# Kernel optimization log

Measured on AMD Instinct MI355X. Metric: run time of the kernel, lower is better.

Reference implementation:

```python
import jax, jax.numpy as jnp
import numpy as np

B, C, H, W = 4, 3, 1024, 1024
RADII = (8, 16, 32, 64)
EPS = 1e-5  # BatchNorm2d default eps


def _box_sum(x, r, s):
    # depthwise all-ones conv (kernel r, stride s, VALID padding) == summed box
    return jax.lax.reduce_window(x, 0.0, jax.lax.add, (1, 1, r, r), (1, 1, s, s), 'VALID')


def _axis_interp_ac(x, n_out, axis):
    # bilinear (align_corners=True) interpolation along one axis
    n_in = x.shape[axis]
    pos = jnp.arange(n_out, dtype=x.dtype) * ((n_in - 1) / max(n_out - 1, 1))
    i0 = jnp.clip(jnp.floor(pos).astype(jnp.int32), 0, n_in - 2)
    w = pos - i0.astype(x.dtype)
    a = jnp.take(x, i0, axis=axis)
    b = jnp.take(x, i0 + 1, axis=axis)
    shape = [1] * x.ndim
    shape[axis] = n_out
    w = w.reshape(shape)
    return a * (1 - w) + b * w


def _resize_ac(x, oh, ow):
    x = _axis_interp_ac(x, oh, 2)
    x = _axis_interp_ac(x, ow, 3)
    return x


def _bn(x, g, b, rm, rv):
    inv = g / jnp.sqrt(rv + EPS)
    return x * inv[None, :, None, None] + (b - rm * inv)[None, :, None, None]


def _forward(guide, src, w1, g1, b1, rm1, rv1, w2, g2, b2, rm2, rv2, w3):
    Hg, Wg = guide.shape[2], guide.shape[3]
    gg = guide * guide
    gs = guide * src
    ones = jnp.ones((1, guide.shape[1], Hg, Wg), guide.dtype)
    stats = []
    for r in RADII:
        s = r // 2
        N = _box_sum(ones, r, s)
        mx = _box_sum(guide, r, s) / N
        my = _box_sum(src, r, s) / N
        cov = _box_sum(gs, r, s) / N - mx * my
        var = _box_sum(gg, r, s) / N - mx * mx
        stats.append((mx, my, cov, var))
    mx1, my1, cov1, var1 = stats[0]
    oh, ow = cov1.shape[2], cov1.shape[3]
    feats = [cov1, var1]
    for (_, _, cov, var) in stats[1:]:
        feats.append(_resize_ac(cov, oh, ow))
        feats.append(_resize_ac(var, oh, ow))
    x = jnp.concatenate(feats, axis=1)  # [B,24,oh,ow]
    x = jax.nn.relu(_bn(jnp.einsum('oc,bchw->bohw', w1, x), g1, b1, rm1, rv1))
    x = jax.nn.relu(_bn(jnp.einsum('oc,bchw->bohw', w2, x), g2, b2, rm2, rv2))
    A = jnp.einsum('oc,bchw->bohw', w3, x)  # [B,3,oh,ow]
    bb = my1 - A * mx1
    mean_A = _resize_ac(A, Hg, Wg)
    mean_b = _resize_ac(bb, Hg, Wg)
    return mean_A * guide + mean_b


def setup_inputs() -> dict:
    key = jax.random.key(0)
    ks = jax.random.split(key, 5)
    f32 = jnp.float32
    return {
        'guide': jax.random.normal(ks[0], (B, C, H, W), f32),
        'src': jax.random.normal(ks[1], (B, C, H, W), f32),
        'w1': jax.random.normal(ks[2], (48, 24), f32) * 0.05,
        'g1': jnp.ones((48,), f32), 'b1': jnp.zeros((48,), f32),
        'rm1': jnp.zeros((48,), f32), 'rv1': jnp.ones((48,), f32),
        'w2': jax.random.normal(ks[3], (48, 48), f32) * 0.05,
        'g2': jnp.ones((48,), f32), 'b2': jnp.zeros((48,), f32),
        'rm2': jnp.zeros((48,), f32), 'rv2': jnp.ones((48,), f32),
        'w3': jax.random.normal(ks[4], (3, 48), f32) * 0.05,
    }


def reference(guide, src, w1, g1, b1, rm1, rv1, w2, g2, b2, rm2, rv2, w3):
    return _forward(guide, src, w1, g1, b1, rm1, rv1, w2, g2, b2, rm2, rv2, w3)
```

## Files before the change

kernel.cpp:

```cpp
#include <hip/hip_runtime.h>

typedef float v2f __attribute__((ext_vector_type(2)));

#define HH 1024
#define WW 1024
#define NB 4
#define NC 3
#define BC 12
#define N1 255
#define N2 127
#define N3 63
#define N4 31
#define EPS 1e-5f
#define NPIX (NB * N1 * N1)

constexpr size_t S8_OFF = 0;
constexpr size_t S8_SZ  = 4ull * BC * N1 * N1;
constexpr size_t CV16_OFF = S8_OFF + S8_SZ;
constexpr size_t CV16_SZ  = 2ull * BC * N2 * N2;
constexpr size_t CV32_OFF = CV16_OFF + CV16_SZ;
constexpr size_t CV32_SZ  = 2ull * BC * N3 * N3;
constexpr size_t CV64_OFF = CV32_OFF + CV32_SZ;
constexpr size_t CV64_SZ  = 2ull * BC * N4 * N4;
constexpr size_t AB_OFF = CV64_OFF + CV64_SZ;
constexpr size_t AB_SZ  = 2ull * NB * NC * N1 * N1;
constexpr size_t IB_OFF = AB_OFF + AB_SZ;

__global__ __launch_bounds__(256) void base_kernel(
    const float* __restrict__ guide, const float* __restrict__ src,
    float4* __restrict__ S8q)
{
    __shared__ float smem[8][WW];

    int b  = blockIdx.x % 64;
    int bc = blockIdx.x / 64;
    int t  = threadIdx.x;

    const float* gbase = guide + (size_t)bc * HH * WW + 4 * t;
    const float* sbase = src   + (size_t)bc * HH * WW + 4 * t;

    auto load_grp = [&](int g, float c[4][4]) {
#pragma unroll
        for (int q = 0; q < 4; ++q)
#pragma unroll
            for (int k = 0; k < 4; ++k) c[q][k] = 0.f;
#pragma unroll
        for (int r = 0; r < 4; ++r) {
            int row = 16 * b + 4 * g + r;
            if (row < HH) {
                float4 g4 = *(const float4*)(gbase + (size_t)row * WW);
                float4 s4 = *(const float4*)(sbase + (size_t)row * WW);
                float ge[4] = {g4.x, g4.y, g4.z, g4.w};
                float se[4] = {s4.x, s4.y, s4.z, s4.w};
#pragma unroll
                for (int k = 0; k < 4; ++k) {
                    c[0][k] += ge[k];
                    c[1][k] += se[k];
                    c[2][k] += ge[k] * ge[k];
                    c[3][k] += ge[k] * se[k];
                }
            }
        }
    };

    auto store_combo = [&](int rowsel, const float a[4][4], const float bb[4][4]) {
#pragma unroll
        for (int q = 0; q < 4; ++q) {
            float4 v;
            v.x = a[q][0] + bb[q][0];
            v.y = a[q][1] + bb[q][1];
            v.z = a[q][2] + bb[q][2];
            v.w = a[q][3] + bb[q][3];
            *(float4*)&smem[rowsel * 4 + q][4 * t] = v;
        }
    };

    auto emit = [&](int rowsel, int i) {
        if (t < N1 && i < N1) {
            float qv[4];
#pragma unroll
            for (int q = 0; q < 4; ++q) {
                const float* arr = smem[rowsel * 4 + q];
                float4 a4 = *(const float4*)(arr + 4 * t);
                float4 b4 = *(const float4*)(arr + 4 * t + 4);
                qv[q] = (a4.x + a4.y) + (a4.z + a4.w) +
                        (b4.x + b4.y) + (b4.z + b4.w);
            }
            float4 o4; o4.x = qv[0]; o4.y = qv[1]; o4.z = qv[2]; o4.w = qv[3];
            S8q[(size_t)bc * N1 * N1 + (size_t)i * N1 + t] = o4;
        }
    };

    float c0[4][4], c1[4][4], c2[4][4];
    load_grp(0, c0);
    load_grp(1, c1);
    load_grp(2, c2);
    store_combo(0, c0, c1);
    store_combo(1, c1, c2);
    __syncthreads();
    emit(0, 4 * b + 0);
    emit(1, 4 * b + 1);
    __syncthreads();
    load_grp(3, c1);
    load_grp(4, c0);
    store_combo(0, c2, c1);
    store_combo(1, c1, c0);
    __syncthreads();
    emit(0, 4 * b + 2);
    emit(1, 4 * b + 3);
}

__global__ __launch_bounds__(256) void pyr_all(
    const float4* __restrict__ S8q, v2f* __restrict__ CV16,
    v2f* __restrict__ CV32, v2f* __restrict__ CV64,
    const float* __restrict__ g1, const float* __restrict__ b1,
    const float* __restrict__ rm1, const float* __restrict__ rv1,
    const float* __restrict__ g2, const float* __restrict__ b2,
    const float* __restrict__ rm2, const float* __restrict__ rv2,
    float* __restrict__ invbia)
{
    if (blockIdx.x == 0 && threadIdx.x < 48) {
        int o = threadIdx.x;
        float iv = g1[o] * rsqrtf(rv1[o] + EPS);
        invbia[o]      = iv;
        invbia[48 + o] = b1[o] - rm1[o] * iv;
        float iv2 = g2[o] * rsqrtf(rv2[o] + EPS);
        invbia[96 + o]  = iv2;
        invbia[144 + o] = b2[o] - rm2[o] * iv2;
    }

    const int n2t = BC * N2 * N2, n3t = BC * N3 * N3, n4t = BC * N4 * N4;
    int idx = blockIdx.x * 256 + threadIdx.x;

    v2f* CV; int nout, cnt; float invN; int rem;
    if (idx < n2t)              { CV = CV16; nout = N2; cnt = 2; invN = 1.f / 256.f;  rem = idx; }
    else if (idx < n2t + n3t)   { CV = CV32; nout = N3; cnt = 4; invN = 1.f / 1024.f; rem = idx - n2t; }
    else if (idx < n2t + n3t + n4t) { CV = CV64; nout = N4; cnt = 8; invN = 1.f / 4096.f; rem = idx - n2t - n3t; }
    else return;

    int j  = rem % nout;
    int tt = rem / nout;
    int i  = tt % nout;
    int bc = tt / nout;

    const float4* P = S8q + (size_t)bc * N1 * N1;
    int p0 = cnt * i, q0 = cnt * j;

    float s0 = 0.f, s1 = 0.f, s2 = 0.f, s3 = 0.f;
    for (int ky = 0; ky < cnt; ++ky) {
        size_t roff = (size_t)(p0 + 2 * ky) * N1 + q0;
        for (int kx = 0; kx < cnt; ++kx) {
            float4 q4 = P[roff + 2 * kx];
            s0 += q4.x; s1 += q4.y; s2 += q4.z; s3 += q4.w;
        }
    }

    size_t o = (size_t)bc * nout * nout + (size_t)i * nout + j;
    float mx = s0 * invN, my = s1 * invN;
    v2f cv; cv[0] = s3 * invN - mx * my; cv[1] = s2 * invN - mx * mx;
    CV[o] = cv;
}

__global__ __launch_bounds__(256) void mlp_kernel(
    const float4* __restrict__ S8q,
    const v2f* __restrict__ CV16, const v2f* __restrict__ CV32,
    const v2f* __restrict__ CV64,
    const float* __restrict__ w1, const float* __restrict__ w2,
    const float* __restrict__ w3, const float* __restrict__ invbia,
    v2f* __restrict__ AB)
{
    int idx = blockIdx.x * 256 + threadIdx.x;
    if (idx >= NPIX) return;
    int ox = idx % N1;
    int r  = idx / N1;
    int oy = r % N1;
    int b  = r / N1;

    float feats[24], mx1[3], my1[3];

#pragma unroll
    for (int c = 0; c < 3; ++c) {
        float4 q4 = S8q[(size_t)(b * 3 + c) * N1 * N1 + (size_t)oy * N1 + ox];
        float mx = q4.x * (1.f / 64.f), my = q4.y * (1.f / 64.f);
        mx1[c] = mx; my1[c] = my;
        feats[c]     = q4.w * (1.f / 64.f) - mx * my;
        feats[3 + c] = q4.z * (1.f / 64.f) - mx * mx;
    }

    const v2f* CVs[3]   = {CV16, CV32, CV64};
    const int nins[3]   = {N2, N3, N4};
    const float scales[3] = {(float)(126.0 / 254.0), (float)(62.0 / 254.0),
                             (float)(30.0 / 254.0)};
#pragma unroll
    for (int l = 0; l < 3; ++l) {
        const v2f* CV = CVs[l];
        int nin = nins[l];
        float sc = scales[l];
        float py = (float)oy * sc;
        int   i0 = min(max((int)floorf(py), 0), nin - 2);
        float wy = py - (float)i0;
        float px = (float)ox * sc;
        int   j0 = min(max((int)floorf(px), 0), nin - 2);
        float wx = px - (float)j0;
        int fo = 6 + 6 * l;
#pragma unroll
        for (int c = 0; c < 3; ++c) {
            size_t o00 = (size_t)(b * 3 + c) * nin * nin + (size_t)i0 * nin + j0;
            v2f c00 = CV[o00], c01 = CV[o00 + 1];
            v2f c10 = CV[o00 + nin], c11 = CV[o00 + nin + 1];
            v2f res = (c00 * (1.f - wy) + c10 * wy) * (1.f - wx) +
                      (c01 * (1.f - wy) + c11 * wy) * wx;
            feats[fo + c]     = res[0];
            feats[fo + 3 + c] = res[1];
        }
    }

    v2f f2[12];
#pragma unroll
    for (int k = 0; k < 12; ++k) { f2[k][0] = feats[2 * k]; f2[k][1] = feats[2 * k + 1]; }

    v2f h1v[24];
#pragma unroll
    for (int o = 0; o < 48; ++o) {
        v2f acc = {0.f, 0.f};
#pragma unroll
        for (int k = 0; k < 12; ++k) {
            v2f wv = *(const v2f*)(w1 + o * 24 + 2 * k);
            acc += wv * f2[k];
        }
        float v = fmaxf((acc[0] + acc[1]) * invbia[o] + invbia[48 + o], 0.f);
        h1v[o >> 1][o & 1] = v;
    }
    v2f h2v[24];
#pragma unroll
    for (int o = 0; o < 48; ++o) {
        v2f acc = {0.f, 0.f};
#pragma unroll
        for (int k = 0; k < 24; ++k) {
            v2f wv = *(const v2f*)(w2 + o * 48 + 2 * k);
            acc += wv * h1v[k];
        }
        float v = fmaxf((acc[0] + acc[1]) * invbia[96 + o] + invbia[144 + o], 0.f);
        h2v[o >> 1][o & 1] = v;
    }
#pragma unroll
    for (int c = 0; c < 3; ++c) {
        v2f acc = {0.f, 0.f};
#pragma unroll
        for (int k = 0; k < 24; ++k) {
            v2f wv = *(const v2f*)(w3 + c * 48 + 2 * k);
            acc += wv * h2v[k];
        }
        float a = acc[0] + acc[1];
        v2f ab; ab[0] = a; ab[1] = my1[c] - a * mx1[c];
        AB[(size_t)(b * 3 + c) * N1 * N1 + (size_t)oy * N1 + ox] = ab;
    }
}

__global__ __launch_bounds__(256) void final_kernel(
    const float* __restrict__ guide, const v2f* __restrict__ AB,
    float* __restrict__ out)
{
    __shared__ v2f abH[N1 + 1];
    int blk = blockIdx.x;
    int bc  = blk / HH;
    int h   = blk % HH;

    const float scale = (float)(254.0 / 1023.0);
    float py = (float)h * scale;
    int   i0 = min(max((int)floorf(py), 0), N1 - 2);
    float wy = py - (float)i0;

    int t = threadIdx.x;
    if (t < N1) {
        size_t base = (size_t)bc * N1 * N1 + (size_t)i0 * N1 + t;
        v2f p0 = AB[base], p1 = AB[base + N1];
        abH[t] = p0 * (1.f - wy) + p1 * wy;
    }
    __syncthreads();

    const float* gp = guide + (size_t)bc * HH * WW + (size_t)h * WW;
    float*       op = out   + (size_t)bc * HH * WW + (size_t)h * WW;

    float4 g4 = *(const float4*)(gp + 4 * t);
    float ge[4] = {g4.x, g4.y, g4.z, g4.w};
    float oe[4];
#pragma unroll
    for (int k = 0; k < 4; ++k) {
        int w = 4 * t + k;
        float px = (float)w * scale;
        int   j0 = min(max((int)floorf(px), 0), N1 - 2);
        float wx = px - (float)j0;
        v2f ab = abH[j0] * (1.f - wx) + abH[j0 + 1] * wx;
        oe[k] = ab[0] * ge[k] + ab[1];
    }
    float4 o4; o4.x = oe[0]; o4.y = oe[1]; o4.z = oe[2]; o4.w = oe[3];
    *(float4*)(op + 4 * t) = o4;
}

extern "C" void kernel_launch(void* const* d_in, const int* in_sizes, int n_in,
                              void* d_out, int out_size, void* d_ws, size_t ws_size,
                              hipStream_t stream)
{
    const float* guide = (const float*)d_in[0];
    const float* src   = (const float*)d_in[1];
    const float* w1    = (const float*)d_in[2];
    const float* g1    = (const float*)d_in[3];
    const float* b1    = (const float*)d_in[4];
    const float* rm1   = (const float*)d_in[5];
    const float* rv1   = (const float*)d_in[6];
    const float* w2    = (const float*)d_in[7];
    const float* g2    = (const float*)d_in[8];
    const float* b2    = (const float*)d_in[9];
    const float* rm2   = (const float*)d_in[10];
    const float* rv2   = (const float*)d_in[11];
    const float* w3    = (const float*)d_in[12];
    float*       out   = (float*)d_out;

    float* ws    = (float*)d_ws;
    float4* S8q  = (float4*)(ws + S8_OFF);
    v2f*   CV16  = (v2f*)(ws + CV16_OFF);
    v2f*   CV32  = (v2f*)(ws + CV32_OFF);
    v2f*   CV64  = (v2f*)(ws + CV64_OFF);
    v2f*   AB    = (v2f*)(ws + AB_OFF);
    float* invbia = ws + IB_OFF;

    base_kernel<<<BC * 64, 256, 0, stream>>>(guide, src, S8q);

    {
        int total = BC * (N2 * N2 + N3 * N3 + N4 * N4);
        pyr_all<<<(total + 255) / 256, 256, 0, stream>>>(
            S8q, CV16, CV32, CV64, g1, b1, rm1, rv1, g2, b2, rm2, rv2, invbia);
    }

    mlp_kernel<<<(NPIX + 255) / 256, 256, 0, stream>>>(
        S8q, CV16, CV32, CV64, w1, w2, w3, invbia, AB);

    final_kernel<<<BC * HH, 256, 0, stream>>>(guide, AB, out);
}
```

Measured before the change: 245.1 us.

## Tile MLP kernel 16x16 with LDS-staged pyramid patches and weights

The MLP kernel now processes 16x16 output tiles per block and stages the needed coarse-level covariance/variance patches, w1, and the packed BN scale/bias into shared memory, so bilinear gathers read LDS instead of global memory. The weight loops switch to float4 loads, and the w2/w3 pointers are offset by (tid & zero) with zero passed as 0, which keeps the compiler from treating those loads as uniform scalar loads. The h2 loop is only partially unrolled to limit register pressure. The cost is extra shared memory, a block barrier, and more index arithmetic for the tile origins.

```diff
diff --git a/kernel.cpp b/kernel.cpp
--- a/kernel.cpp
+++ b/kernel.cpp
@@ -117,16 +117,16 @@
     const float* __restrict__ rm1, const float* __restrict__ rv1,
     const float* __restrict__ g2, const float* __restrict__ b2,
     const float* __restrict__ rm2, const float* __restrict__ rv2,
-    float* __restrict__ invbia)
+    v2f* __restrict__ ibv)
 {
     if (blockIdx.x == 0 && threadIdx.x < 48) {
         int o = threadIdx.x;
         float iv = g1[o] * rsqrtf(rv1[o] + EPS);
-        invbia[o]      = iv;
-        invbia[48 + o] = b1[o] - rm1[o] * iv;
+        v2f p1; p1[0] = iv; p1[1] = b1[o] - rm1[o] * iv;
+        ibv[o] = p1;
         float iv2 = g2[o] * rsqrtf(rv2[o] + EPS);
-        invbia[96 + o]  = iv2;
-        invbia[144 + o] = b2[o] - rm2[o] * iv2;
+        v2f p2; p2[0] = iv2; p2[1] = b2[o] - rm2[o] * iv2;
+        ibv[48 + o] = p2;
     }
 
     const int n2t = BC * N2 * N2, n3t = BC * N3 * N3, n4t = BC * N4 * N4;
@@ -166,15 +166,58 @@
     const v2f* __restrict__ CV16, const v2f* __restrict__ CV32,
     const v2f* __restrict__ CV64,
     const float* __restrict__ w1, const float* __restrict__ w2,
-    const float* __restrict__ w3, const float* __restrict__ invbia,
-    v2f* __restrict__ AB)
+    const float* __restrict__ w3, const v2f* __restrict__ ibv,
+    v2f* __restrict__ AB, int zero)
 {
-    int idx = blockIdx.x * 256 + threadIdx.x;
-    if (idx >= NPIX) return;
-    int ox = idx % N1;
-    int r  = idx / N1;
-    int oy = r % N1;
-    int b  = r / N1;
+    __shared__ float4 sw1q[288];
+    __shared__ v2f    sib[96];
+    __shared__ v2f    s2[3 * 100];
+    __shared__ v2f    s3[3 * 36];
+    __shared__ v2f    s4[3 * 16];
+
+    const float scl2 = (float)(126.0 / 254.0);
+    const float scl3 = (float)(62.0 / 254.0);
+    const float scl4 = (float)(30.0 / 254.0);
+
+    int tid  = threadIdx.x;
+    int tile = blockIdx.x;
+    int b    = tile >> 8;
+    int t2   = tile & 255;
+    int ty0  = (t2 >> 4) * 16;
+    int tx0  = (t2 & 15) * 16;
+
+    int bi2 = min(max((int)floorf((float)ty0 * scl2), 0), N2 - 2);
+    int bj2 = min(max((int)floorf((float)tx0 * scl2), 0), N2 - 2);
+    int bi3 = min(max((int)floorf((float)ty0 * scl3), 0), N3 - 2);
+    int bj3 = min(max((int)floorf((float)tx0 * scl3), 0), N3 - 2);
+    int bi4 = min(max((int)floorf((float)ty0 * scl4), 0), N4 - 2);
+    int bj4 = min(max((int)floorf((float)tx0 * scl4), 0), N4 - 2);
+
+    {
+        const float4* w1q = (const float4*)w1;
+        for (int k = tid; k < 288; k += 256) sw1q[k] = w1q[k];
+        if (tid < 96) sib[tid] = ibv[tid];
+        for (int k = tid; k < 300; k += 256) {
+            int ch = k / 100, idx = k % 100, r = idx / 10, c = idx % 10;
+            int sr = min(bi2 + r, N2 - 1), sc = min(bj2 + c, N2 - 1);
+            s2[k] = CV16[(size_t)(b * 3 + ch) * N2 * N2 + (size_t)sr * N2 + sc];
+        }
+        if (tid < 108) {
+            int ch = tid / 36, idx = tid % 36, r = idx / 6, c = idx % 6;
+            int sr = min(bi3 + r, N3 - 1), sc = min(bj3 + c, N3 - 1);
+            s3[tid] = CV32[(size_t)(b * 3 + ch) * N3 * N3 + (size_t)sr * N3 + sc];
+        }
+        if (tid < 48) {
+            int ch = tid / 16, idx = tid % 16, r = idx / 4, c = idx % 4;
+            int sr = min(bi4 + r, N4 - 1), sc = min(bj4 + c, N4 - 1);
+            s4[tid] = CV64[(size_t)(b * 3 + ch) * N4 * N4 + (size_t)sr * N4 + sc];
+        }
+    }
+    __syncthreads();
+
+    int dy = tid >> 4, dx = tid & 15;
+    int oy = ty0 + dy, ox = tx0 + dx;
+    if (oy >= N1 || ox >= N1) return;
 
     float feats[24], mx1[3], my1[3];
 
@@ -187,31 +230,37 @@
         feats[3 + c] = q4.z * (1.f / 64.f) - mx * mx;
     }
 
-    const v2f* CVs[3]   = {CV16, CV32, CV64};
-    const int nins[3]   = {N2, N3, N4};
-    const float scales[3] = {(float)(126.0 / 254.0), (float)(62.0 / 254.0),
-                             (float)(30.0 / 254.0)};
-#pragma unroll
-    for (int l = 0; l < 3; ++l) {
-        const v2f* CV = CVs[l];
-        int nin = nins[l];
-        float sc = scales[l];
-        float py = (float)oy * sc;
-        int   i0 = min(max((int)floorf(py), 0), nin - 2);
-        float wy = py - (float)i0;
-        float px = (float)ox * sc;
-        int   j0 = min(max((int)floorf(px), 0), nin - 2);
-        float wx = px - (float)j0;
-        int fo = 6 + 6 * l;
-#pragma unroll
-        for (int c = 0; c < 3; ++c) {
-            size_t o00 = (size_t)(b * 3 + c) * nin * nin + (size_t)i0 * nin + j0;
-            v2f c00 = CV[o00], c01 = CV[o00 + 1];
-            v2f c10 = CV[o00 + nin], c11 = CV[o00 + nin + 1];
-            v2f res = (c00 * (1.f - wy) + c10 * wy) * (1.f - wx) +
-                      (c01 * (1.f - wy) + c11 * wy) * wx;
-            feats[fo + c]     = res[0];
-            feats[fo + 3 + c] = res[1];
+    {
+        const v2f* tiles[3] = {s2, s3, s4};
+        const int spans[3]  = {10, 6, 4};
+        const int chsz[3]   = {100, 36, 16};
+        const int nins[3]   = {N2, N3, N4};
+        const float scls[3] = {scl2, scl3, scl4};
+        const int bis[3]    = {bi2, bi3, bi4};
+        const int bjs[3]    = {bj2, bj3, bj4};
+#pragma unroll
+        for (int l = 0; l < 3; ++l) {
+            int nin = nins[l];
+            float sc = scls[l];
+            float py = (float)oy * sc;
+            int   i0 = min(max((int)floorf(py), 0), nin - 2);
+            float wy = py - (float)i0;
+            float px = (float)ox * sc;
+            int   j0 = min(max((int)floorf(px), 0), nin - 2);
+            float wx = px - (float)j0;
+            int r = i0 - bis[l], c = j0 - bjs[l];
+            int span = spans[l];
+            int fo = 6 + 6 * l;
+#pragma unroll
+            for (int ch = 0; ch < 3; ++ch) {
+                const v2f* tp = tiles[l] + ch * chsz[l] + r * span + c;
+                v2f c00 = tp[0], c01 = tp[1];
+                v2f c10 = tp[span], c11 = tp[span + 1];
+                v2f res = (c00 * (1.f - wy) + c10 * wy) * (1.f - wx) +
+                          (c01 * (1.f - wy) + c11 * wy) * wx;
+                feats[fo + ch]     = res[0];
+                feats[fo + 3 + ch] = res[1];
+            }
         }
     }
 
@@ -219,37 +268,50 @@
 #pragma unroll
     for (int k = 0; k < 12; ++k) { f2[k][0] = feats[2 * k]; f2[k][1] = feats[2 * k + 1]; }
 
+    const float4* w2v = (const float4*)w2 + (tid & zero);
+    const float4* w3v = (const float4*)w3 + (tid & zero);
+
     v2f h1v[24];
 #pragma unroll
     for (int o = 0; o < 48; ++o) {
+        const float4* wr = &sw1q[o * 6];
         v2f acc = {0.f, 0.f};
 #pragma unroll
+        for (int k = 0; k < 6; ++k) {
+            float4 wq = wr[k];
+            acc += (v2f){wq.x, wq.y} * f2[2 * k];
+            acc += (v2f){wq.z, wq.w} * f2[2 * k + 1];
+        }
+        v2f ib = sib[o];
+        float v = fmaxf((acc[0] + acc[1]) * ib[0] + ib[1], 0.f);
+        h1v[o >> 1][o & 1] = v;
+    }
+
+    v2f h2v[24];
+#pragma unroll 4
+    for (int o = 0; o < 48; ++o) {
+        const float4* wr = w2v + o * 12;
+        v2f acc = {0.f, 0.f};
+#pragma unroll
         for (int k = 0; k < 12; ++k) {
-            v2f wv = *(const v2f*)(w1 + o * 24 + 2 * k);
-            acc += wv * f2[k];
-        }
-        float v = fmaxf((acc[0] + acc[1]) * invbia[o] + invbia[48 + o], 0.f);
-        h1v[o >> 1][o & 1] = v;
-    }
-    v2f h2v[24];
-#pragma unroll
-    for (int o = 0; o < 48; ++o) {
+            float4 wq = wr[k];
+            acc += (v2f){wq.x, wq.y} * h1v[2 * k];
+            acc += (v2f){wq.z, wq.w} * h1v[2 * k + 1];
+        }
+        v2f ib = sib[48 + o];
+        float v = fmaxf((acc[0] + acc[1]) * ib[0] + ib[1], 0.f);
+        h2v[o >> 1][o & 1] = v;
+    }
+
+#pragma unroll
+    for (int c = 0; c < 3; ++c) {
+        const float4* wr = w3v + c * 12;
         v2f acc = {0.f, 0.f};
 #pragma unroll
-        for (int k = 0; k < 24; ++k) {
-            v2f wv = *(const v2f*)(w2 + o * 48 + 2 * k);
-            acc += wv * h1v[k];
-        }
-        float v = fmaxf((acc[0] + acc[1]) * invbia[96 + o] + invbia[144 + o], 0.f);
-        h2v[o >> 1][o & 1] = v;
-    }
-#pragma unroll
-    for (int c = 0; c < 3; ++c) {
-        v2f acc = {0.f, 0.f};
-#pragma unroll
-        for (int k = 0; k < 24; ++k) {
-            v2f wv = *(const v2f*)(w3 + c * 48 + 2 * k);
-            acc += wv * h2v[k];
+        for (int k = 0; k < 12; ++k) {
+            float4 wq = wr[k];
+            acc += (v2f){wq.x, wq.y} * h2v[2 * k];
+            acc += (v2f){wq.z, wq.w} * h2v[2 * k + 1];
         }
         float a = acc[0] + acc[1];
         v2f ab; ab[0] = a; ab[1] = my1[c] - a * mx1[c];
@@ -323,18 +385,18 @@
     v2f*   CV32  = (v2f*)(ws + CV32_OFF);
     v2f*   CV64  = (v2f*)(ws + CV64_OFF);
     v2f*   AB    = (v2f*)(ws + AB_OFF);
-    float* invbia = ws + IB_OFF;
+    v2f*   ibv   = (v2f*)(ws + IB_OFF);
 
     base_kernel<<<BC * 64, 256, 0, stream>>>(guide, src, S8q);
 
     {
         int total = BC * (N2 * N2 + N3 * N3 + N4 * N4);
         pyr_all<<<(total + 255) / 256, 256, 0, stream>>>(
-            S8q, CV16, CV32, CV64, g1, b1, rm1, rv1, g2, b2, rm2, rv2, invbia);
-    }
-
-    mlp_kernel<<<(NPIX + 255) / 256, 256, 0, stream>>>(
-        S8q, CV16, CV32, CV64, w1, w2, w3, invbia, AB);
+            S8q, CV16, CV32, CV64, g1, b1, rm1, rv1, g2, b2, rm2, rv2, ibv);
+    }
+
+    mlp_kernel<<<NB * 256, 256, 0, stream>>>(
+        S8q, CV16, CV32, CV64, w1, w2, w3, ibv, AB, 0);
 
     final_kernel<<<BC * HH, 256, 0, stream>>>(guide, AB, out);
 }
```

After: 309.7 us. 1.26x slower.
